# Performance work log

Measured on AMD Instinct MI355X. Metric: run time of the kernel, lower is better.

The kernel has to match this reference:

```python
import jax, jax.numpy as jnp
import numpy as np

CODEBOOK_SIZE = 32768
EMBED_DIM = 4


def setup_inputs() -> dict:
    key = jax.random.key(0)
    k1, k2 = jax.random.split(key)
    # [batch, temporal, channels, height, width]
    hidden_state = jax.random.normal(k1, (1, 4, EMBED_DIM, 48, 48), dtype=jnp.float32)
    # nn.Embedding weight, init uniform(-1/cb, 1/cb) as in the torch module
    embedding = jax.random.uniform(
        k2, (CODEBOOK_SIZE, EMBED_DIM), dtype=jnp.float32,
        minval=-1.0 / CODEBOOK_SIZE, maxval=1.0 / CODEBOOK_SIZE,
    )
    return {"hidden_state": hidden_state, "embedding": embedding}


def reference(hidden_state, embedding):
    b, t, c, h, w = hidden_state.shape
    # permute channels last, flatten to [N, C]
    x = jnp.transpose(hidden_state, (0, 1, 3, 4, 2)).reshape(-1, c)
    distances = (
        jnp.sum(x * x, axis=1, keepdims=True)
        + jnp.sum(embedding * embedding, axis=1)
        - 2.0 * jnp.einsum("nd,kd->nk", x, embedding)
    )
    min_encoding_indices = jnp.argmin(distances, axis=1)
    return min_encoding_indices.reshape(b, t, h, w)
```

## Files before the change

### kernel.cpp

```cpp
#include <hip/hip_runtime.h>
#include <cfloat>


#define ROWS   9
#define BLOCK  256
#define NK     32768
#define EPT    4
#define CHUNK  (BLOCK * EPT)

__global__ __launch_bounds__(BLOCK, 4)
void vq_argmin_kernel(const float* __restrict__ hs,
                      const float4* __restrict__ cb,
                      int* __restrict__ out)
{
    __shared__ float sRD[4 * ROWS];
    __shared__ int   sRI[4 * ROWS];

    const int tid = threadIdx.x;
    const int rowbase = blockIdx.x * ROWS;

    float xr0[ROWS], xr1[ROWS], xr2[ROWS], xr3[ROWS];
    float x2[ROWS];
    float best[ROWS];
    int   bidx[ROWS];

    #pragma unroll
    for (int r = 0; r < ROWS; ++r) {
        int n = rowbase + r;
        int t = n / 2304;
        int rem = n - t * 2304;
        const float* p = hs + t * 9216 + rem;
        float a0 = p[0], a1 = p[2304], a2 = p[4608], a3 = p[6912];
        xr0[r] = a0; xr1[r] = a1; xr2[r] = a2; xr3[r] = a3;
        x2[r] = __fadd_rn(__fadd_rn(__fadd_rn(__fmul_rn(a0, a0),
                                              __fmul_rn(a1, a1)),
                                    __fmul_rn(a2, a2)),
                          __fmul_rn(a3, a3));
        best[r] = FLT_MAX;
        bidx[r] = 0;
    }

    float4 ce[EPT], ne[EPT];
    #pragma unroll
    for (int j = 0; j < EPT; ++j) ce[j] = cb[tid + j * BLOCK];

    for (int tb = 0; tb < NK; tb += CHUNK) {
        int nb = tb + CHUNK < NK ? tb + CHUNK : tb;
        #pragma unroll
        for (int j = 0; j < EPT; ++j) ne[j] = cb[nb + tid + j * BLOCK];

        #pragma unroll
        for (int j = 0; j < EPT; ++j) {
            float4 e = ce[j];
            float e2v = __fadd_rn(__fadd_rn(__fadd_rn(__fmul_rn(e.x, e.x),
                                                      __fmul_rn(e.y, e.y)),
                                            __fmul_rn(e.z, e.z)),
                                  __fmul_rn(e.w, e.w));
            int kk = tb + tid + j * BLOCK;
            #pragma unroll
            for (int r = 0; r < ROWS; ++r) {
                float dot = __builtin_fmaf(xr3[r], e.w,
                            __builtin_fmaf(xr2[r], e.z,
                            __builtin_fmaf(xr1[r], e.y,
                            __fmul_rn(xr0[r], e.x))));
                float t1 = __fadd_rn(x2[r], e2v);
                float d  = __builtin_fmaf(dot, -2.0f, t1);
                if (d < best[r]) { best[r] = d; bidx[r] = kk; }
            }
        }

        #pragma unroll
        for (int j = 0; j < EPT; ++j) ce[j] = ne[j];
    }

    #pragma unroll
    for (int r = 0; r < ROWS; ++r) {
        float d = best[r]; int i = bidx[r];
        #pragma unroll
        for (int off = 32; off >= 1; off >>= 1) {
            float d2 = __shfl_xor(d, off, 64);
            int   i2 = __shfl_xor(i, off, 64);
            if (d2 < d || (d2 == d && i2 < i)) { d = d2; i = i2; }
        }
        best[r] = d; bidx[r] = i;
    }

    int wave = tid >> 6;
    if ((tid & 63) == 0) {
        #pragma unroll
        for (int r = 0; r < ROWS; ++r) {
            sRD[wave * ROWS + r] = best[r];
            sRI[wave * ROWS + r] = bidx[r];
        }
    }
    __syncthreads();

    if (tid < ROWS) {
        float d = sRD[tid]; int i = sRI[tid];
        #pragma unroll
        for (int w = 1; w < 4; ++w) {
            float d2 = sRD[w * ROWS + tid];
            int   i2 = sRI[w * ROWS + tid];
            if (d2 < d || (d2 == d && i2 < i)) { d = d2; i = i2; }
        }
        out[rowbase + tid] = i;
    }
}

extern "C" void kernel_launch(void* const* d_in, const int* in_sizes, int n_in,
                              void* d_out, int out_size, void* d_ws, size_t ws_size,
                              hipStream_t stream)
{
    const float*  hs = (const float*)d_in[0];
    const float4* cb = (const float4*)d_in[1];
    int* out = (int*)d_out;

    const int nrows = 9216;
    dim3 grid(nrows / ROWS), block(BLOCK);
    vq_argmin_kernel<<<grid, block, 0, stream>>>(hs, cb, out);
}
```

Measured before the change: 126.8 us.

## Stage codebook slabs in LDS via async global_load_lds with more rows per block

Each block now handles 36 rows instead of 9, using 512 threads. The codebook is streamed through double-buffered LDS slabs filled by async global_load_lds, and the query rows are read from shared memory in chunks of 12. This cuts the number of blocks (256 instead of 1024) and the total codebook traffic per row, and reuses each codebook element across more rows. The cost is a sync per slab, LDS reads of x inside the loop, higher register pressure from 36 best/index pairs, and only 256 blocks to fill the GPU.

New measurement: 163.5 us. 1.29x slower.

```diff
diff --git a/kernel.cpp b/kernel.cpp
--- a/kernel.cpp
+++ b/kernel.cpp
@@ -2,75 +2,97 @@
 #include <cfloat>
 
 
-#define ROWS   9
-#define BLOCK  256
-#define NK     32768
-#define EPT    4
-#define CHUNK  (BLOCK * EPT)
+#define BLOCK  512
+#define ROWS   36
+#define RC     12
+#define NCH    (ROWS / RC)
+#define SLAB   1024
+#define NSLAB  (32768 / SLAB)
+#define EPT    (SLAB / BLOCK)
 
-__global__ __launch_bounds__(BLOCK, 4)
+typedef const __attribute__((address_space(1))) void GAS;
+typedef __attribute__((address_space(3))) void LAS;
+
+__global__ __launch_bounds__(BLOCK, 2)
 void vq_argmin_kernel(const float* __restrict__ hs,
                       const float4* __restrict__ cb,
                       int* __restrict__ out)
 {
-    __shared__ float sRD[4 * ROWS];
-    __shared__ int   sRI[4 * ROWS];
+    __shared__ float4 buf[2][SLAB];
+    __shared__ float4 sX4[ROWS];
+    __shared__ float  sX1[ROWS];
 
     const int tid = threadIdx.x;
     const int rowbase = blockIdx.x * ROWS;
 
-    float xr0[ROWS], xr1[ROWS], xr2[ROWS], xr3[ROWS];
-    float x2[ROWS];
-    float best[ROWS];
-    int   bidx[ROWS];
+    #pragma unroll
+    for (int j = 0; j < EPT; ++j) {
+        int slot = j * BLOCK + tid;
+        __builtin_amdgcn_global_load_lds((GAS*)(cb + slot),
+                                         (LAS*)(&buf[0][slot]), 16, 0, 0);
+    }
 
-    #pragma unroll
-    for (int r = 0; r < ROWS; ++r) {
-        int n = rowbase + r;
+    if (tid < ROWS) {
+        int n = rowbase + tid;
         int t = n / 2304;
         int rem = n - t * 2304;
         const float* p = hs + t * 9216 + rem;
         float a0 = p[0], a1 = p[2304], a2 = p[4608], a3 = p[6912];
-        xr0[r] = a0; xr1[r] = a1; xr2[r] = a2; xr3[r] = a3;
-        x2[r] = __fadd_rn(__fadd_rn(__fadd_rn(__fmul_rn(a0, a0),
-                                              __fmul_rn(a1, a1)),
-                                    __fmul_rn(a2, a2)),
-                          __fmul_rn(a3, a3));
-        best[r] = FLT_MAX;
-        bidx[r] = 0;
+        sX4[tid] = make_float4(a0, a1, a2, a3);
+        sX1[tid] = __fadd_rn(__fadd_rn(__fadd_rn(__fmul_rn(a0, a0),
+                                                 __fmul_rn(a1, a1)),
+                                       __fmul_rn(a2, a2)),
+                             __fmul_rn(a3, a3));
     }
 
-    float4 ce[EPT], ne[EPT];
+    float best[ROWS];
+    int   bidx[ROWS];
     #pragma unroll
-    for (int j = 0; j < EPT; ++j) ce[j] = cb[tid + j * BLOCK];
+    for (int r = 0; r < ROWS; ++r) { best[r] = FLT_MAX; bidx[r] = 0; }
 
-    for (int tb = 0; tb < NK; tb += CHUNK) {
-        int nb = tb + CHUNK < NK ? tb + CHUNK : tb;
-        #pragma unroll
-        for (int j = 0; j < EPT; ++j) ne[j] = cb[nb + tid + j * BLOCK];
-
-        #pragma unroll
-        for (int j = 0; j < EPT; ++j) {
-            float4 e = ce[j];
-            float e2v = __fadd_rn(__fadd_rn(__fadd_rn(__fmul_rn(e.x, e.x),
-                                                      __fmul_rn(e.y, e.y)),
-                                            __fmul_rn(e.z, e.z)),
-                                  __fmul_rn(e.w, e.w));
-            int kk = tb + tid + j * BLOCK;
+    for (int s = 0; s < NSLAB; ++s) {
+        __syncthreads();
+        if (s + 1 < NSLAB) {
+            const float4* src = cb + (s + 1) * SLAB;
             #pragma unroll
-            for (int r = 0; r < ROWS; ++r) {
-                float dot = __builtin_fmaf(xr3[r], e.w,
-                            __builtin_fmaf(xr2[r], e.z,
-                            __builtin_fmaf(xr1[r], e.y,
-                            __fmul_rn(xr0[r], e.x))));
-                float t1 = __fadd_rn(x2[r], e2v);
-                float d  = __builtin_fmaf(dot, -2.0f, t1);
-                if (d < best[r]) { best[r] = d; bidx[r] = kk; }
+            for (int j = 0; j < EPT; ++j) {
+                int slot = j * BLOCK + tid;
+                __builtin_amdgcn_global_load_lds((GAS*)(src + slot),
+                                                 (LAS*)(&buf[(s + 1) & 1][slot]),
+                                                 16, 0, 0);
             }
         }
-
+        const float4* sb = buf[s & 1];
+        int kbase = s * SLAB + tid;
         #pragma unroll
-        for (int j = 0; j < EPT; ++j) ce[j] = ne[j];
+        for (int c = 0; c < NCH; ++c) {
+            float4 xr[RC]; float xq[RC];
+            #pragma unroll
+            for (int r = 0; r < RC; ++r) {
+                xr[r] = sX4[c * RC + r];
+                xq[r] = sX1[c * RC + r];
+            }
+            #pragma unroll
+            for (int j = 0; j < EPT; ++j) {
+                float4 e = sb[j * BLOCK + tid];
+                float e2 = __fadd_rn(__fadd_rn(__fadd_rn(__fmul_rn(e.x, e.x),
+                                                         __fmul_rn(e.y, e.y)),
+                                               __fmul_rn(e.z, e.z)),
+                                     __fmul_rn(e.w, e.w));
+                int kk = kbase + j * BLOCK;
+                #pragma unroll
+                for (int r = 0; r < RC; ++r) {
+                    float dot = __builtin_fmaf(xr[r].w, e.w,
+                                __builtin_fmaf(xr[r].z, e.z,
+                                __builtin_fmaf(xr[r].y, e.y,
+                                __fmul_rn(xr[r].x, e.x))));
+                    float t1 = __fadd_rn(xq[r], e2);
+                    float d  = __builtin_fmaf(dot, -2.0f, t1);
+                    int idx = c * RC + r;
+                    if (d < best[idx]) { best[idx] = d; bidx[idx] = kk; }
+                }
+            }
+        }
     }
 
     #pragma unroll
@@ -85,22 +107,26 @@
         best[r] = d; bidx[r] = i;
     }
 
+    __syncthreads();
+    float* rd = (float*)&buf[0][0];
+    int*   ri = (int*)(rd + 8 * ROWS);
+
     int wave = tid >> 6;
     if ((tid & 63) == 0) {
         #pragma unroll
         for (int r = 0; r < ROWS; ++r) {
-            sRD[wave * ROWS + r] = best[r];
-            sRI[wave * ROWS + r] = bidx[r];
+            rd[wave * ROWS + r] = best[r];
+            ri[wave * ROWS + r] = bidx[r];
         }
     }
     __syncthreads();
 
     if (tid < ROWS) {
-        float d = sRD[tid]; int i = sRI[tid];
+        float d = rd[tid]; int i = ri[tid];
         #pragma unroll
-        for (int w = 1; w < 4; ++w) {
-            float d2 = sRD[w * ROWS + tid];
-            int   i2 = sRI[w * ROWS + tid];
+        for (int w = 1; w < 8; ++w) {
+            float d2 = rd[w * ROWS + tid];
+            int   i2 = ri[w * ROWS + tid];
             if (d2 < d || (d2 == d && i2 < i)) { d = d2; i = i2; }
         }
         out[rowbase + tid] = i;
@@ -115,7 +141,6 @@
     const float4* cb = (const float4*)d_in[1];
     int* out = (int*)d_out;
 
-    const int nrows = 9216;
-    dim3 grid(nrows / ROWS), block(BLOCK);
+    dim3 grid(9216 / ROWS), block(BLOCK);
     vq_argmin_kernel<<<grid, block, 0, stream>>>(hs, cb, out);
 }
```
